# Kernel tuning notes

Measured on AMD Instinct MI355X. Metric: run time of the kernel, lower is better.

Reference implementation:

```python
import jax, jax.numpy as jnp
import numpy as np

LAMBDA_E_SUM = 10.0
LAMBDA_HIT = 20.0
LAMBDA_CHAMFER = 1e-3
LAMBDA_HIT_ENTROPY = 0.1
EPS = 1e-6
BIG = 1e18


def setup_inputs() -> dict:
    key = jax.random.key(0)
    ks = jax.random.split(key, 7)
    B, Np, Ng, L = 32, 2048, 2048, 256
    pred_feat = jax.random.normal(ks[0], (B, 4, Np), dtype=jnp.float32)
    # hit-probability channel must be in (0,1) (sigmoid head in the real model)
    pred_hit = jax.random.uniform(ks[1], (B, 1, Np), dtype=jnp.float32,
                                  minval=1e-4, maxval=1.0 - 1e-4)
    preds = jnp.concatenate([pred_feat, pred_hit], axis=1)          # [B,5,Np]
    target = jax.random.normal(ks[2], (B, 4, Ng), dtype=jnp.float32)  # [B,4,Ng]
    target_mask = (jax.random.uniform(ks[3], (B, Ng)) < 0.9).astype(jnp.float32)
    mu = jax.random.normal(ks[4], (B, L), dtype=jnp.float32)
    logvar = 0.5 * jax.random.normal(ks[5], (B, L), dtype=jnp.float32)
    e_init = jax.random.uniform(ks[6], (B,), dtype=jnp.float32,
                                minval=10.0, maxval=100.0)
    kl_weight = jnp.float32(1e-3)
    return {"preds": preds, "target": target, "target_mask": target_mask,
            "mu": mu, "logvar": logvar, "e_init": e_init,
            "kl_weight": kl_weight}


def reference(preds, target, target_mask, mu, logvar, e_init, kl_weight):
    B = preds.shape[0]
    preds_t = jnp.swapaxes(preds, 1, 2)    # [B, Np, 5]
    target_t = jnp.swapaxes(target, 1, 2)  # [B, Ng, 4]
    pred_xyz = preds_t[..., :3]            # [B, Np, 3]
    pred_E = preds_t[..., 3]               # [B, Np]
    pred_hit = preds_t[..., 4]             # [B, Np]
    target_xyz = target_t[..., :3]         # [B, Ng, 3]
    target_E = target_t[..., 3]            # [B, Ng]

    # squared pairwise distances [B, Np, Ng]
    pn = jnp.sum(pred_xyz * pred_xyz, axis=-1)      # [B, Np]
    tn = jnp.sum(target_xyz * target_xyz, axis=-1)  # [B, Ng]
    dist_sq = jnp.maximum(
        pn[:, :, None] + tn[:, None, :]
        - 2.0 * jnp.einsum('bnd,bmd->bnm', pred_xyz, target_xyz), 0.0)

    inf_mask = target_mask[:, None, :] == 0.0       # [B, 1->Np, Ng]
    dist_sq_masked = jnp.where(inf_mask, BIG, dist_sq)
    min_dist_pred = jnp.min(dist_sq_masked, axis=2)     # [B, Np]
    idx_pred = jnp.argmin(dist_sq_masked, axis=2)       # [B, Np]
    min_dist_target = jnp.min(dist_sq, axis=1)          # [B, Ng]

    mask_sum = jnp.sum(target_mask)
    loss_chamfer_target = jnp.sum(min_dist_target * target_mask) / mask_sum
    loss_chamfer_pred = jnp.mean(min_dist_pred)
    loss_chamfer = loss_chamfer_target + loss_chamfer_pred

    matched_target_E = jnp.take_along_axis(target_E, idx_pred, axis=1)  # [B, Np]
    loss_local_E = jnp.mean(jnp.abs(pred_E - matched_target_E))

    n_hits_pred = jnp.sum(pred_hit, axis=1)                 # [B]
    n_hits_target = jnp.sum(target_mask, axis=1)            # [B]
    loss_hit_count = jnp.mean((n_hits_pred - n_hits_target) ** 2)

    loss_hit_entropy = -jnp.mean(pred_hit * jnp.log(pred_hit + EPS)
                                 + (1.0 - pred_hit) * jnp.log(1.0 - pred_hit + EPS))

    total_pred_E = jnp.sum(pred_E * pred_hit, axis=1)       # [B]
    loss_global_E_sum = jnp.mean((total_pred_E - e_init) ** 2)

    loss_kld = -0.5 * jnp.sum(1.0 + logvar - mu * mu - jnp.exp(logvar)) / B

    loss_chamf = loss_chamfer * LAMBDA_CHAMFER
    losskld = kl_weight * loss_kld
    loss_global_e = LAMBDA_E_SUM * loss_global_E_sum
    loss_hit = LAMBDA_HIT * loss_hit_count
    loss_hit_entr = LAMBDA_HIT_ENTROPY * loss_hit_entropy

    total_loss = (loss_chamf + loss_local_E + losskld
                  + loss_global_e + loss_hit + loss_hit_entr)
    components = jnp.stack([loss_chamf, loss_local_E, loss_global_e,
                            loss_hit, losskld])
    return total_loss, components
```

## Files before the change

kernel.cpp:

```cpp
#include <hip/hip_runtime.h>

#define BB 32
#define NP 2048
#define NG 2048
#define EPSF 1e-6f
#define BIGF 1e18f
#define FLTMAX 3.4e38f
#define MT 128
#define MP 16
#define TPT 4

#define FPART_OFF 0
#define PPART_OFF 65536
#define TPART_OFF (65536 + BB * MP * NP * 8)

__global__ __launch_bounds__(256, 8) void k_pair(const float* __restrict__ preds,
                                                 const float* __restrict__ target,
                                                 const float* __restrict__ mask,
                                                 unsigned long long* __restrict__ ppart,
                                                 float* __restrict__ tpart) {
  __shared__ float4 s4[MT];
  const int bx = blockIdx.x;
  const int tid = threadIdx.x;

  if (bx < 1024) {
    const int b = bx >> 5;
    const int nch = (bx >> 4) & 1;
    const int mp = bx & 15;
    const float* tb = target + b * 4 * NG;
    const int mbase = mp * MT;
    if (tid < MT) {
      int m = mbase + tid;
      float tx = tb[m], ty = tb[NG + m], tz = tb[2 * NG + m];
      float tn = fmaf(tx, tx, fmaf(ty, ty, tz * tz));
      float w = tn + (mask[b * NG + m] == 0.0f ? BIGF : 0.0f);
      s4[tid] = make_float4(-2.0f * tx, -2.0f * ty, -2.0f * tz, w);
    }
    __syncthreads();

    const float* pb = preds + b * 5 * NP;
    const int nbase = nch * 1024 + tid;
    float px[TPT], py[TPT], pz[TPT], bv[TPT];
    int bi[TPT];
#pragma unroll
    for (int k = 0; k < TPT; k++) {
      int n = nbase + k * 256;
      px[k] = pb[n];
      py[k] = pb[NP + n];
      pz[k] = pb[2 * NP + n];
      bv[k] = FLTMAX;
      bi[k] = 0;
    }

#pragma unroll 4
    for (int m = 0; m < MT; m++) {
      float4 t = s4[m];
#pragma unroll
      for (int k = 0; k < TPT; k++) {
        float s = fmaf(px[k], t.x, fmaf(py[k], t.y, fmaf(pz[k], t.z, t.w)));
        if (s < bv[k]) { bv[k] = s; bi[k] = m; }
      }
    }

    unsigned long long* row = &ppart[(b * MP + mp) * NP];
#pragma unroll
    for (int k = 0; k < TPT; k++) {
      float pn = fmaf(px[k], px[k], fmaf(py[k], py[k], pz[k] * pz[k]));
      float d = fmaxf(bv[k] + pn, 0.0f);
      row[nbase + k * 256] =
          ((unsigned long long)__float_as_uint(d) << 32) | (unsigned)(mbase + bi[k]);
    }
  } else {
    const int bb = bx - 1024;
    const int b = bb >> 5;
    const int mch = (bb >> 4) & 1;
    const int np_ = bb & 15;
    const float* pb = preds + b * 5 * NP;
    if (tid < MT) {
      int n = np_ * MT + tid;
      float px = pb[n], py = pb[NP + n], pz = pb[2 * NP + n];
      float pn2 = fmaf(px, px, fmaf(py, py, pz * pz));
      s4[tid] = make_float4(-2.0f * px, -2.0f * py, -2.0f * pz, pn2);
    }
    __syncthreads();

    const float* tb = target + b * 4 * NG;
    const int mbase2 = mch * 1024 + tid;
    float tx[TPT], ty[TPT], tz[TPT], cv[TPT];
#pragma unroll
    for (int k = 0; k < TPT; k++) {
      int m = mbase2 + k * 256;
      tx[k] = tb[m];
      ty[k] = tb[NG + m];
      tz[k] = tb[2 * NG + m];
      cv[k] = FLTMAX;
    }

#pragma unroll 4
    for (int n = 0; n < MT; n++) {
      float4 p = s4[n];
#pragma unroll
      for (int k = 0; k < TPT; k++)
        cv[k] = fminf(cv[k], fmaf(tx[k], p.x, fmaf(ty[k], p.y, fmaf(tz[k], p.z, p.w))));
    }

    float* row = &tpart[(b * MP + np_) * NG];
#pragma unroll
    for (int k = 0; k < TPT; k++) {
      float tn = fmaf(tx[k], tx[k], fmaf(ty[k], ty[k], tz[k] * tz[k]));
      row[mbase2 + k * 256] = fmaxf(cv[k] + tn, 0.0f);
    }
  }
}

__global__ __launch_bounds__(256) void k_fin(const unsigned long long* __restrict__ ppart,
                                             const float* __restrict__ tpart,
                                             const float* __restrict__ preds,
                                             const float* __restrict__ target,
                                             const float* __restrict__ mask,
                                             const float* __restrict__ mu,
                                             const float* __restrict__ logvar,
                                             float* __restrict__ fpart) {
  __shared__ float red[4][8];
  const int bx = blockIdx.x;
  const int tid = threadIdx.x;
  const int wave = tid >> 6, lane = tid & 63;
  float q0 = 0.0f, q1 = 0.0f, q2 = 0.0f, q3 = 0.0f, q4 = 0.0f;

  if (bx < 128) {
    const int b = bx >> 2;
    const float* pb = preds + b * 5 * NP;
    const float* te = target + b * 4 * NG + 3 * NG;
#pragma unroll
    for (int e = 0; e < 2; e++) {
      int i = bx * 512 + e * 256 + tid;
      int n = i & 2047;
      unsigned long long best = 0xFFFFFFFFFFFFFFFFull;
      const unsigned long long* col = &ppart[b * MP * NP + n];
#pragma unroll
      for (int mp = 0; mp < MP; mp++) {
        unsigned long long v = col[mp * NP];
        best = v < best ? v : best;
      }
      float bd = __uint_as_float((unsigned)(best >> 32));
      int idx = (int)(best & 0xffffffffu);
      float mE = te[idx];
      float pE = pb[3 * NP + n];
      float ph = pb[4 * NP + n];
      q0 += bd;
      q1 += fabsf(pE - mE);
      q2 += ph * logf(ph + EPSF) + (1.0f - ph) * logf(1.0f - ph + EPSF);
      q3 += ph;
      q4 += pE * ph;
    }
  } else if (bx < 256) {
    const int bb = bx - 128;
    const int b = bb >> 2;
#pragma unroll
    for (int e = 0; e < 2; e++) {
      int i = bb * 512 + e * 256 + tid;
      int m = i & 2047;
      float d = FLTMAX;
      const float* col = &tpart[b * MP * NG + m];
#pragma unroll
      for (int np_ = 0; np_ < MP; np_++) d = fminf(d, col[np_ * NG]);
      float msk = mask[i];
      q0 += d * msk;
      q1 += msk;
      q2 += msk;
    }
  } else {
    const int bb = bx - 256;
#pragma unroll
    for (int e = 0; e < 4; e++) {
      int i = bb * 1024 + e * 256 + tid;
      float m = mu[i], lv = logvar[i];
      q0 += 1.0f + lv - m * m - expf(lv);
    }
  }

  float qs[5] = {q0, q1, q2, q3, q4};
  for (int k = 0; k < 5; k++) {
    float v = qs[k];
    v += __shfl_down(v, 32);
    v += __shfl_down(v, 16);
    v += __shfl_down(v, 8);
    v += __shfl_down(v, 4);
    v += __shfl_down(v, 2);
    v += __shfl_down(v, 1);
    if (lane == 0) red[wave][k] = v;
  }
  __syncthreads();
  if (tid < 5) fpart[bx * 8 + tid] = red[0][tid] + red[1][tid] + red[2][tid] + red[3][tid];
}

__global__ __launch_bounds__(256) void k_final(const float* __restrict__ fpart,
                                               const float* __restrict__ e_init,
                                               const float* __restrict__ kl_weight,
                                               float* __restrict__ out) {
  __shared__ float red[4][8];
  const int t = threadIdx.x;
  const int wave = t >> 6, lane = t & 63;
  float g[8] = {0, 0, 0, 0, 0, 0, 0, 0};
  if (t < 128) {
    const float* r = &fpart[t * 8];
    g[0] = r[0]; g[1] = r[1]; g[2] = r[2];
    const float* r2 = &fpart[(128 + t) * 8];
    g[3] = r2[0]; g[4] = r2[1];
  }
  if (t < 8) g[5] = fpart[(256 + t) * 8];
  if (t < BB) {
    float hit = 0.0f, eh = 0.0f, mk = 0.0f;
#pragma unroll
    for (int k = 0; k < 4; k++) {
      hit += fpart[(4 * t + k) * 8 + 3];
      eh += fpart[(4 * t + k) * 8 + 4];
      mk += fpart[(128 + 4 * t + k) * 8 + 2];
    }
    float dh = hit - mk;
    g[6] = dh * dh;
    float de = eh - e_init[t];
    g[7] = de * de;
  }
  for (int k = 0; k < 8; k++) {
    float v = g[k];
    v += __shfl_down(v, 32);
    v += __shfl_down(v, 16);
    v += __shfl_down(v, 8);
    v += __shfl_down(v, 4);
    v += __shfl_down(v, 2);
    v += __shfl_down(v, 1);
    if (lane == 0) red[wave][k] = v;
  }
  __syncthreads();
  if (t == 0) {
    float s[8];
    for (int k = 0; k < 8; k++) s[k] = red[0][k] + red[1][k] + red[2][k] + red[3][k];
    const float invBN = 1.0f / (float)(BB * NP);
    float chamfer_pred = s[0] * invBN;
    float localE = s[1] * invBN;
    float ent = -s[2] * invBN;
    float chamfer_tgt = s[3] / s[4];
    float kld = -0.5f * s[5] / (float)BB;
    float hit = s[6] / (float)BB;
    float ge = s[7] / (float)BB;

    float loss_chamf = (chamfer_tgt + chamfer_pred) * 0.001f;
    float losskld = kl_weight[0] * kld;
    float loss_ge = 10.0f * ge;
    float loss_hit = 20.0f * hit;
    float loss_ent = 0.1f * ent;

    float total = loss_chamf + localE + losskld + loss_ge + loss_hit + loss_ent;
    out[0] = total;
    out[1] = loss_chamf;
    out[2] = localE;
    out[3] = loss_ge;
    out[4] = loss_hit;
    out[5] = losskld;
  }
}

extern "C" void kernel_launch(void* const* d_in, const int* in_sizes, int n_in,
                              void* d_out, int out_size, void* d_ws, size_t ws_size,
                              hipStream_t stream) {
  const float* preds = (const float*)d_in[0];
  const float* target = (const float*)d_in[1];
  const float* mask = (const float*)d_in[2];
  const float* mu = (const float*)d_in[3];
  const float* logvar = (const float*)d_in[4];
  const float* e_init = (const float*)d_in[5];
  const float* kl_weight = (const float*)d_in[6];
  float* fpart = (float*)((char*)d_ws + FPART_OFF);
  unsigned long long* ppart = (unsigned long long*)((char*)d_ws + PPART_OFF);
  float* tpart = (float*)((char*)d_ws + TPART_OFF);
  float* out = (float*)d_out;

  k_pair<<<2048, 256, 0, stream>>>(preds, target, mask, ppart, tpart);
  k_fin<<<264, 256, 0, stream>>>(ppart, tpart, preds, target, mask, mu, logvar, fpart);
  k_final<<<1, 256, 0, stream>>>(fpart, e_init, kl_weight, out);
}
```

Measured before the change: 105.7 us.

## Fuse final reduction into k_fin via last-block atomic counter

Removes the separate single-block k_final launch by having the last k_fin block to finish, found through an atomic counter, perform the global reduction. It uses relaxed agent-scope atomic loads and a threadfence so that block sees the partials written by the others. The counter is reset by k_pair. It also restructures the target-side min loop to process two pred points per iteration with a paired fminf, aiming for more instruction-level parallelism. The cost is an extra atomic and fence in every k_fin block.

```diff
diff --git a/kernel.cpp b/kernel.cpp
--- a/kernel.cpp
+++ b/kernel.cpp
@@ -11,17 +11,25 @@
 #define TPT 4
 
 #define FPART_OFF 0
+#define CNT_OFF 8448
 #define PPART_OFF 65536
 #define TPART_OFF (65536 + BB * MP * NP * 8)
+
+__device__ __forceinline__ float cload(const float* p) {
+  return __hip_atomic_load(p, __ATOMIC_RELAXED, __HIP_MEMORY_SCOPE_AGENT);
+}
 
 __global__ __launch_bounds__(256, 8) void k_pair(const float* __restrict__ preds,
                                                  const float* __restrict__ target,
                                                  const float* __restrict__ mask,
                                                  unsigned long long* __restrict__ ppart,
-                                                 float* __restrict__ tpart) {
+                                                 float* __restrict__ tpart,
+                                                 unsigned* __restrict__ cnt) {
   __shared__ float4 s4[MT];
   const int bx = blockIdx.x;
   const int tid = threadIdx.x;
+
+  if (bx == 0 && tid == 0) *cnt = 0;
 
   if (bx < 1024) {
     const int b = bx >> 5;
@@ -96,12 +104,16 @@
       cv[k] = FLTMAX;
     }
 
-#pragma unroll 4
-    for (int n = 0; n < MT; n++) {
-      float4 p = s4[n];
-#pragma unroll
-      for (int k = 0; k < TPT; k++)
-        cv[k] = fminf(cv[k], fmaf(tx[k], p.x, fmaf(ty[k], p.y, fmaf(tz[k], p.z, p.w))));
+#pragma unroll 2
+    for (int n = 0; n < MT; n += 2) {
+      float4 p0 = s4[n];
+      float4 p1 = s4[n + 1];
+#pragma unroll
+      for (int k = 0; k < TPT; k++) {
+        float s0 = fmaf(tx[k], p0.x, fmaf(ty[k], p0.y, fmaf(tz[k], p0.z, p0.w)));
+        float s1 = fmaf(tx[k], p1.x, fmaf(ty[k], p1.y, fmaf(tz[k], p1.z, p1.w)));
+        cv[k] = fminf(cv[k], fminf(s0, s1));
+      }
     }
 
     float* row = &tpart[(b * MP + np_) * NG];
@@ -120,8 +132,13 @@
                                              const float* __restrict__ mask,
                                              const float* __restrict__ mu,
                                              const float* __restrict__ logvar,
-                                             float* __restrict__ fpart) {
+                                             const float* __restrict__ e_init,
+                                             const float* __restrict__ kl_weight,
+                                             float* __restrict__ fpart,
+                                             unsigned* __restrict__ cnt,
+                                             float* __restrict__ out) {
   __shared__ float red[4][8];
+  __shared__ int s_last;
   const int bx = blockIdx.x;
   const int tid = threadIdx.x;
   const int wave = tid >> 6, lane = tid & 63;
@@ -192,34 +209,37 @@
   }
   __syncthreads();
   if (tid < 5) fpart[bx * 8 + tid] = red[0][tid] + red[1][tid] + red[2][tid] + red[3][tid];
-}
-
-__global__ __launch_bounds__(256) void k_final(const float* __restrict__ fpart,
-                                               const float* __restrict__ e_init,
-                                               const float* __restrict__ kl_weight,
-                                               float* __restrict__ out) {
-  __shared__ float red[4][8];
-  const int t = threadIdx.x;
-  const int wave = t >> 6, lane = t & 63;
+
+  __syncthreads();
+  if (tid == 0) {
+    __threadfence();
+    s_last = (atomicAdd(cnt, 1u) == 263u) ? 1 : 0;
+  }
+  __syncthreads();
+  if (!s_last) return;
+
   float g[8] = {0, 0, 0, 0, 0, 0, 0, 0};
-  if (t < 128) {
-    const float* r = &fpart[t * 8];
-    g[0] = r[0]; g[1] = r[1]; g[2] = r[2];
-    const float* r2 = &fpart[(128 + t) * 8];
-    g[3] = r2[0]; g[4] = r2[1];
-  }
-  if (t < 8) g[5] = fpart[(256 + t) * 8];
-  if (t < BB) {
+  if (tid < 128) {
+    const float* r = fpart + tid * 8;
+    g[0] = cload(r + 0);
+    g[1] = cload(r + 1);
+    g[2] = cload(r + 2);
+    const float* r2 = fpart + (128 + tid) * 8;
+    g[3] = cload(r2 + 0);
+    g[4] = cload(r2 + 1);
+  }
+  if (tid < 8) g[5] = cload(fpart + (256 + tid) * 8);
+  if (tid < BB) {
     float hit = 0.0f, eh = 0.0f, mk = 0.0f;
 #pragma unroll
     for (int k = 0; k < 4; k++) {
-      hit += fpart[(4 * t + k) * 8 + 3];
-      eh += fpart[(4 * t + k) * 8 + 4];
-      mk += fpart[(128 + 4 * t + k) * 8 + 2];
+      hit += cload(fpart + (4 * tid + k) * 8 + 3);
+      eh += cload(fpart + (4 * tid + k) * 8 + 4);
+      mk += cload(fpart + (128 + 4 * tid + k) * 8 + 2);
     }
     float dh = hit - mk;
     g[6] = dh * dh;
-    float de = eh - e_init[t];
+    float de = eh - e_init[tid];
     g[7] = de * de;
   }
   for (int k = 0; k < 8; k++) {
@@ -233,7 +253,7 @@
     if (lane == 0) red[wave][k] = v;
   }
   __syncthreads();
-  if (t == 0) {
+  if (tid == 0) {
     float s[8];
     for (int k = 0; k < 8; k++) s[k] = red[0][k] + red[1][k] + red[2][k] + red[3][k];
     const float invBN = 1.0f / (float)(BB * NP);
@@ -272,11 +292,12 @@
   const float* e_init = (const float*)d_in[5];
   const float* kl_weight = (const float*)d_in[6];
   float* fpart = (float*)((char*)d_ws + FPART_OFF);
+  unsigned* cnt = (unsigned*)((char*)d_ws + CNT_OFF);
   unsigned long long* ppart = (unsigned long long*)((char*)d_ws + PPART_OFF);
   float* tpart = (float*)((char*)d_ws + TPART_OFF);
   float* out = (float*)d_out;
 
-  k_pair<<<2048, 256, 0, stream>>>(preds, target, mask, ppart, tpart);
-  k_fin<<<264, 256, 0, stream>>>(ppart, tpart, preds, target, mask, mu, logvar, fpart);
-  k_final<<<1, 256, 0, stream>>>(fpart, e_init, kl_weight, out);
+  k_pair<<<2048, 256, 0, stream>>>(preds, target, mask, ppart, tpart, cnt);
+  k_fin<<<264, 256, 0, stream>>>(ppart, tpart, preds, target, mask, mu, logvar,
+                                 e_init, kl_weight, fpart, cnt, out);
 }
```

Result: no change. 105.3 us (-0.4%).
